# Optimization experiments

Hardware: AMD Instinct MI355X
Metric: run time of the kernel (lower is better)

Reference implementation:

```python
import jax, jax.numpy as jnp
import numpy as np

N, T, F, H, E, L = 50000, 12, 2, 64, 800000, 2


def setup_inputs() -> dict:
    key = jax.random.key(0)
    ks = jax.random.split(key, 8)
    x = jax.random.normal(ks[0], (N, T, F), jnp.float32)
    h0 = jnp.zeros((L, N, H), jnp.float32)
    edge_index = jax.random.randint(ks[1], (2, E), 0, N)
    edge_weight = jax.random.uniform(ks[2], (E,), jnp.float32)
    def glorot(k, shape):
        fan = shape[0]
        return jax.random.normal(k, shape, jnp.float32) / np.sqrt(fan).astype(np.float32)
    Wg0 = glorot(ks[3], (F + H, 2 * H)); bg0 = jnp.zeros((2 * H,), jnp.float32)
    Wc0 = glorot(ks[4], (F + H, H));     bc0 = jnp.zeros((H,), jnp.float32)
    Wg1 = glorot(ks[5], (H + H, 2 * H)); bg1 = jnp.zeros((2 * H,), jnp.float32)
    Wc1 = glorot(ks[6], (H + H, H));     bc1 = jnp.zeros((H,), jnp.float32)
    return dict(x=x, h0=h0, edge_index=edge_index, edge_weight=edge_weight,
                Wg0=Wg0, bg0=bg0, Wc0=Wc0, bc0=bc0,
                Wg1=Wg1, bg1=bg1, Wc1=Wc1, bc1=bc1)


def reference(x, h0, edge_index, edge_weight, Wg0, bg0, Wc0, bc0, Wg1, bg1, Wc1, bc1):
    n = x.shape[0]
    src, dst = edge_index[0], edge_index[1]

    def gcn(f, W, b):
        # weighted gather from src nodes, scatter-add into dst nodes, then linear
        agg = jax.ops.segment_sum(edge_weight[:, None] * f[src], dst, num_segments=n)
        return agg @ W + b

    def layer(inputs, h_init, Wg, bg, Wc, bc):
        def step(h, x_t):
            cat = jnp.concatenate([x_t, h], axis=-1)            # [N, F+H]
            zr = jax.nn.sigmoid(gcn(cat, Wg, bg))               # [N, 2H]
            z, r = jnp.split(zr, 2, axis=-1)
            cand = jnp.tanh(gcn(jnp.concatenate([x_t, r * h], axis=-1), Wc, bc))
            h_new = z * h + (1.0 - z) * cand
            return h_new, h_new
        hT, outs = jax.lax.scan(step, h_init, jnp.swapaxes(inputs, 0, 1))  # outs: [T, N, H]
        return hT, jnp.swapaxes(outs, 0, 1)                                # [N, T, H]

    h1, out1 = layer(x, h0[0], Wg0, bg0, Wc0, bc0)
    h2, out2 = layer(out1, h0[1], Wg1, bg1, Wc1, bc1)
    return jnp.stack([h1, h2], axis=0), out2
```

## Files before the change

### kernel.cpp

```cpp
#include <hip/hip_runtime.h>
#include <hip/hip_bf16.h>

#define DEV __device__ __forceinline__

DEV float4 ld4(const float* p) { return *reinterpret_cast<const float4*>(p); }
DEV float sigmoidf_(float x) { return 1.f / (1.f + expf(-x)); }

DEV void fma8(float (&a)[8], float xv, float4 wa, float4 wb) {
  a[0] = fmaf(xv, wa.x, a[0]); a[1] = fmaf(xv, wa.y, a[1]);
  a[2] = fmaf(xv, wa.z, a[2]); a[3] = fmaf(xv, wa.w, a[3]);
  a[4] = fmaf(xv, wb.x, a[4]); a[5] = fmaf(xv, wb.y, a[5]);
  a[6] = fmaf(xv, wb.z, a[6]); a[7] = fmaf(xv, wb.w, a[7]);
}
DEV void fma4(float (&a)[4], float xv, float4 wa) {
  a[0] = fmaf(xv, wa.x, a[0]); a[1] = fmaf(xv, wa.y, a[1]);
  a[2] = fmaf(xv, wa.z, a[2]); a[3] = fmaf(xv, wa.w, a[3]);
}
DEV float4 wfma4(float4 a, float w, float4 r) {
  a.x = __fadd_rn(a.x, __fmul_rn(w, r.x));
  a.y = __fadd_rn(a.y, __fmul_rn(w, r.y));
  a.z = __fadd_rn(a.z, __fmul_rn(w, r.z));
  a.w = __fadd_rn(a.w, __fmul_rn(w, r.w));
  return a;
}


__global__ void count_kernel(const int* __restrict__ dst, int* __restrict__ cnt, int E) {
  int e = blockIdx.x * blockDim.x + threadIdx.x;
  if (e < E) atomicAdd(&cnt[dst[e]], 1);
}

__global__ __launch_bounds__(256) void blockreduce_kernel(const int* __restrict__ cnt,
                                                          int* __restrict__ bsum, int n) {
  int i = blockIdx.x * 256 + threadIdx.x;
  int v = (i < n) ? cnt[i] : 0;
#pragma unroll
  for (int d = 1; d < 64; d <<= 1) v += __shfl_xor(v, d, 64);
  __shared__ int sh[4];
  if ((threadIdx.x & 63) == 0) sh[threadIdx.x >> 6] = v;
  __syncthreads();
  if (threadIdx.x == 0) bsum[blockIdx.x] = sh[0] + sh[1] + sh[2] + sh[3];
}

__global__ __launch_bounds__(256) void scanb_kernel(const int* __restrict__ bsum,
                                                    int* __restrict__ boff, int nb) {
  __shared__ int sh[256];
  int t = threadIdx.x;
  int orig = (t < nb) ? bsum[t] : 0;
  int v = orig;
  sh[t] = v;
  __syncthreads();
  for (int d = 1; d < 256; d <<= 1) {
    int a = (t >= d) ? sh[t - d] : 0;
    __syncthreads();
    v += a;
    sh[t] = v;
    __syncthreads();
  }
  if (t < nb) boff[t] = v - orig;
}

__global__ __launch_bounds__(256) void blockscan_kernel(
    const int* __restrict__ cnt, const int* __restrict__ boff,
    int* __restrict__ off, int* __restrict__ cur, int n, int total) {
  __shared__ int sh[256];
  int b = blockIdx.x, t = threadIdx.x;
  int i = b * 256 + t;
  int orig = (i < n) ? cnt[i] : 0;
  int v = orig;
  sh[t] = v;
  __syncthreads();
  for (int d = 1; d < 256; d <<= 1) {
    int a = (t >= d) ? sh[t - d] : 0;
    __syncthreads();
    v += a;
    sh[t] = v;
    __syncthreads();
  }
  int excl = v - orig + boff[b];
  if (i < n) { off[i] = excl; cur[i] = excl; }
  if (i == n - 1) off[n] = total;
}

__global__ void scatter_kernel(const int* __restrict__ dstI, int* __restrict__ cur,
                               int* __restrict__ eidx, int E) {
  int e = blockIdx.x * blockDim.x + threadIdx.x;
  if (e < E) {
    int p = atomicAdd(&cur[dstI[e]], 1);
    eidx[p] = e;
  }
}

__global__ __launch_bounds__(256) void sortseg_kernel(
    const int* __restrict__ off, int* __restrict__ eidx,
    const int* __restrict__ srcI, const float* __restrict__ ew,
    int2* __restrict__ cse, int n) {
  int node = blockIdx.x * 4 + (threadIdx.x >> 6);
  int lane = threadIdx.x & 63;
  if (node >= n) return;
  int s = off[node], e = off[node + 1];
  int deg = e - s;
  if (deg <= 0) return;
  if (deg <= 64) {
    int v = (lane < deg) ? eidx[s + lane] : 2147483647;
    int rank = 0;
    for (int m = 0; m < 64; ++m) {
      int u = __shfl(v, m, 64);
      rank += (u < v) ? 1 : 0;
    }
    if (lane < deg)
      cse[s + rank] = make_int2(srcI[v], __float_as_int(ew[v]));
  } else if (lane == 0) {
    for (int i = s + 1; i < e; ++i) {
      int key = eidx[i]; int j = i - 1;
      while (j >= s && eidx[j] > key) { eidx[j + 1] = eidx[j]; --j; }
      eidx[j + 1] = key;
    }
    for (int i = s; i < e; ++i) {
      int v = eidx[i];
      cse[i] = make_int2(srcI[v], __float_as_int(ew[v]));
    }
  }
}

__global__ __launch_bounds__(256) void aggx0_kernel(
    const int* __restrict__ off, const int2* __restrict__ cse,
    const float* __restrict__ x, float* __restrict__ ax, int n) {
  int node = blockIdx.x * 8 + (threadIdx.x >> 5);
  int lane = threadIdx.x & 31;
  if (node >= n || lane >= 24) return;
  float a = 0.f;
  int s = off[node], e = off[node + 1];
  int i = s;
  for (; i + 3 < e; i += 4) {
    int2 p0 = cse[i], p1 = cse[i + 1], p2 = cse[i + 2], p3 = cse[i + 3];
    float r0 = x[(size_t)p0.x * 24 + lane];
    float r1 = x[(size_t)p1.x * 24 + lane];
    float r2 = x[(size_t)p2.x * 24 + lane];
    float r3 = x[(size_t)p3.x * 24 + lane];
    a = __fadd_rn(a, __fmul_rn(__int_as_float(p0.y), r0));
    a = __fadd_rn(a, __fmul_rn(__int_as_float(p1.y), r1));
    a = __fadd_rn(a, __fmul_rn(__int_as_float(p2.y), r2));
    a = __fadd_rn(a, __fmul_rn(__int_as_float(p3.y), r3));
  }
  for (; i < e; ++i) {
    int2 p = cse[i];
    a = __fadd_rn(a, __fmul_rn(__int_as_float(p.y), x[(size_t)p.x * 24 + lane]));
  }
  ax[(size_t)node * 24 + lane] = a;
}


__global__ __launch_bounds__(256) void agg1_kernel(
    const int* __restrict__ off, const int2* __restrict__ cse,
    const float* __restrict__ f0, float* __restrict__ o0, int n) {
  const int node = blockIdx.x * 16 + (threadIdx.x >> 4);
  const int g4   = (threadIdx.x & 15) * 4;
  if (node >= n) return;
  int s = off[node], e = off[node + 1];
  float4 acc = make_float4(0.f, 0.f, 0.f, 0.f);
  int i = s;
  if (i + 3 < e) {
    int2 q0 = cse[i], q1 = cse[i + 1], q2 = cse[i + 2], q3 = cse[i + 3];
    for (; i + 7 < e; i += 4) {
      float4 r0 = ld4(f0 + (size_t)q0.x * 64 + g4);
      float4 r1 = ld4(f0 + (size_t)q1.x * 64 + g4);
      float4 r2 = ld4(f0 + (size_t)q2.x * 64 + g4);
      float4 r3 = ld4(f0 + (size_t)q3.x * 64 + g4);
      int2 m0 = cse[i + 4], m1 = cse[i + 5], m2 = cse[i + 6], m3 = cse[i + 7];
      acc = wfma4(acc, __int_as_float(q0.y), r0);
      acc = wfma4(acc, __int_as_float(q1.y), r1);
      acc = wfma4(acc, __int_as_float(q2.y), r2);
      acc = wfma4(acc, __int_as_float(q3.y), r3);
      q0 = m0; q1 = m1; q2 = m2; q3 = m3;
    }
    float4 r0 = ld4(f0 + (size_t)q0.x * 64 + g4);
    float4 r1 = ld4(f0 + (size_t)q1.x * 64 + g4);
    float4 r2 = ld4(f0 + (size_t)q2.x * 64 + g4);
    float4 r3 = ld4(f0 + (size_t)q3.x * 64 + g4);
    acc = wfma4(acc, __int_as_float(q0.y), r0);
    acc = wfma4(acc, __int_as_float(q1.y), r1);
    acc = wfma4(acc, __int_as_float(q2.y), r2);
    acc = wfma4(acc, __int_as_float(q3.y), r3);
    i += 4;
  }
  for (; i < e; ++i) {
    int2 p = cse[i];
    acc = wfma4(acc, __int_as_float(p.y), ld4(f0 + (size_t)p.x * 64 + g4));
  }
  *reinterpret_cast<float4*>(o0 + (size_t)node * 64 + g4) = acc;
}

__global__ __launch_bounds__(256) void agg2_kernel(
    const int* __restrict__ off, const int2* __restrict__ cse,
    const float* __restrict__ f0, float* __restrict__ o0,
    const float* __restrict__ f1, float* __restrict__ o1, int n) {
  const int node = blockIdx.x * 16 + (threadIdx.x >> 4);
  const int g4   = (threadIdx.x & 15) * 4;
  if (node >= n) return;
  int s = off[node], e = off[node + 1];
  float4 a0 = make_float4(0.f, 0.f, 0.f, 0.f);
  float4 a1 = a0;
  int i = s;
  if (i + 3 < e) {
    int2 q0 = cse[i], q1 = cse[i + 1], q2 = cse[i + 2], q3 = cse[i + 3];
    for (; i + 7 < e; i += 4) {
      size_t o0_ = (size_t)q0.x * 64 + g4, o1_ = (size_t)q1.x * 64 + g4;
      size_t o2_ = (size_t)q2.x * 64 + g4, o3_ = (size_t)q3.x * 64 + g4;
      float4 x0 = ld4(f0 + o0_), h0 = ld4(f1 + o0_);
      float4 x1 = ld4(f0 + o1_), h1 = ld4(f1 + o1_);
      float4 x2 = ld4(f0 + o2_), h2 = ld4(f1 + o2_);
      float4 x3 = ld4(f0 + o3_), h3 = ld4(f1 + o3_);
      int2 m0 = cse[i + 4], m1 = cse[i + 5], m2 = cse[i + 6], m3 = cse[i + 7];
      float w0 = __int_as_float(q0.y), w1 = __int_as_float(q1.y);
      float w2 = __int_as_float(q2.y), w3 = __int_as_float(q3.y);
      a0 = wfma4(a0, w0, x0); a1 = wfma4(a1, w0, h0);
      a0 = wfma4(a0, w1, x1); a1 = wfma4(a1, w1, h1);
      a0 = wfma4(a0, w2, x2); a1 = wfma4(a1, w2, h2);
      a0 = wfma4(a0, w3, x3); a1 = wfma4(a1, w3, h3);
      q0 = m0; q1 = m1; q2 = m2; q3 = m3;
    }
    size_t o0_ = (size_t)q0.x * 64 + g4, o1_ = (size_t)q1.x * 64 + g4;
    size_t o2_ = (size_t)q2.x * 64 + g4, o3_ = (size_t)q3.x * 64 + g4;
    float4 x0 = ld4(f0 + o0_), h0 = ld4(f1 + o0_);
    float4 x1 = ld4(f0 + o1_), h1 = ld4(f1 + o1_);
    float4 x2 = ld4(f0 + o2_), h2 = ld4(f1 + o2_);
    float4 x3 = ld4(f0 + o3_), h3 = ld4(f1 + o3_);
    float w0 = __int_as_float(q0.y), w1 = __int_as_float(q1.y);
    float w2 = __int_as_float(q2.y), w3 = __int_as_float(q3.y);
    a0 = wfma4(a0, w0, x0); a1 = wfma4(a1, w0, h0);
    a0 = wfma4(a0, w1, x1); a1 = wfma4(a1, w1, h1);
    a0 = wfma4(a0, w2, x2); a1 = wfma4(a1, w2, h2);
    a0 = wfma4(a0, w3, x3); a1 = wfma4(a1, w3, h3);
    i += 4;
  }
  for (; i < e; ++i) {
    int2 p = cse[i];
    float w = __int_as_float(p.y);
    size_t ro = (size_t)p.x * 64 + g4;
    a0 = wfma4(a0, w, ld4(f0 + ro));
    a1 = wfma4(a1, w, ld4(f1 + ro));
  }
  *reinterpret_cast<float4*>(o0 + (size_t)node * 64 + g4) = a0;
  *reinterpret_cast<float4*>(o1 + (size_t)node * 64 + g4) = a1;
}


template <int KX>
__global__ __launch_bounds__(256) void gates_kernel(
    const float* __restrict__ aggx, int sx,
    const float* __restrict__ aggh,
    const float* __restrict__ Wg, const float* __restrict__ bg,
    const float* __restrict__ hb, float* __restrict__ zb, float* __restrict__ rhb, int n) {
  __shared__ float wS[(KX + 64) * 128];
  const int t = threadIdx.x;
  {
    float4* d = (float4*)wS;
    const float4* src = (const float4*)Wg;
    const int tot = (KX + 64) * 32;
    for (int idx = t; idx < tot; idx += 256) d[idx] = src[idx];
  }
  __syncthreads();

  const int j0 = (t & 15) * 8;
  const int rb = blockIdx.x * 128 + (t >> 4) * 8;
  if (rb >= n) return;
  const int nr = min(8, n - rb);
  int ro[8];
#pragma unroll
  for (int r = 0; r < 8; ++r) ro[r] = (rb + (r < nr ? r : 0)) * 64;

  float a[8][8];
#pragma unroll
  for (int r = 0; r < 8; ++r)
#pragma unroll
    for (int i = 0; i < 8; ++i) a[r][i] = 0.f;

  {
    const float* Wh = wS + KX * 128;
    for (int k = 0; k < 64; k += 4) {
      float4 f[8];
#pragma unroll
      for (int r = 0; r < 8; ++r) f[r] = ld4(aggh + ro[r] + k);
#pragma unroll
      for (int kk = 0; kk < 4; ++kk) {
        const float* wr = Wh + (k + kk) * 128 + j0;
        float4 wa = ld4(wr), wb = ld4(wr + 4);
#pragma unroll
        for (int r = 0; r < 8; ++r) fma8(a[r], ((const float*)&f[r])[kk], wa, wb);
      }
    }
  }
  if constexpr (KX == 2) {
    float xv[8][2];
#pragma unroll
    for (int r = 0; r < 8; ++r) {
      size_t xo = (size_t)(rb + (r < nr ? r : 0)) * sx;
      xv[r][0] = aggx[xo]; xv[r][1] = aggx[xo + 1];
    }
#pragma unroll
    for (int k = 0; k < 2; ++k) {
      const float* wr = wS + k * 128 + j0;
      float4 wa = ld4(wr), wb = ld4(wr + 4);
#pragma unroll
      for (int r = 0; r < 8; ++r) fma8(a[r], xv[r][k], wa, wb);
    }
  } else {
    for (int k = 0; k < KX; k += 4) {
      float4 f[8];
#pragma unroll
      for (int r = 0; r < 8; ++r) f[r] = ld4(aggx + ro[r] + k);
#pragma unroll
      for (int kk = 0; kk < 4; ++kk) {
        const float* wr = wS + (k + kk) * 128 + j0;
        float4 wa = ld4(wr), wb = ld4(wr + 4);
#pragma unroll
        for (int r = 0; r < 8; ++r) fma8(a[r], ((const float*)&f[r])[kk], wa, wb);
      }
    }
  }
#pragma unroll
  for (int i = 0; i < 8; ++i) {
    int j = j0 + i;
    float b = bg[j];
#pragma unroll
    for (int r = 0; r < 8; ++r) {
      if (r < nr) {
        int row = rb + r;
        float sg = sigmoidf_(a[r][i] + b);
        if (j < 64) {
          zb[(size_t)row * 64 + j] = sg;
        } else {
          int jj = j - 64;
          rhb[(size_t)row * 64 + jj] = __fmul_rn(sg, hb[(size_t)row * 64 + jj]);
        }
      }
    }
  }
}


template <int KX>
__global__ __launch_bounds__(256) void cand_kernel(
    const float* __restrict__ aggx, int sx,
    const float* __restrict__ aggrh,
    const float* __restrict__ Wc, const float* __restrict__ bc,
    const float* __restrict__ zb, float* __restrict__ hb,
    float* __restrict__ outp, int ostride, int n) {
  __shared__ float wS[(KX + 64) * 64];
  const int t = threadIdx.x;
  {
    float4* d = (float4*)wS;
    const float4* src = (const float4*)Wc;
    const int tot = (KX + 64) * 16;
    for (int idx = t; idx < tot; idx += 256) d[idx] = src[idx];
  }
  __syncthreads();

  const int j0 = (t & 15) * 4;
  const int rb = blockIdx.x * 128 + (t >> 4) * 8;
  if (rb >= n) return;
  const int nr = min(8, n - rb);
  int ro[8];
#pragma unroll
  for (int r = 0; r < 8; ++r) ro[r] = (rb + (r < nr ? r : 0)) * 64;

  float a[8][4];
#pragma unroll
  for (int r = 0; r < 8; ++r)
#pragma unroll
    for (int i = 0; i < 4; ++i) a[r][i] = 0.f;

  {
    const float* Wh = wS + KX * 64;
    for (int k = 0; k < 64; k += 4) {
      float4 f[8];
#pragma unroll
      for (int r = 0; r < 8; ++r) f[r] = ld4(aggrh + ro[r] + k);
#pragma unroll
      for (int kk = 0; kk < 4; ++kk) {
        float4 wa = ld4(Wh + (k + kk) * 64 + j0);
#pragma unroll
        for (int r = 0; r < 8; ++r) fma4(a[r], ((const float*)&f[r])[kk], wa);
      }
    }
  }
  if constexpr (KX == 2) {
    float xv[8][2];
#pragma unroll
    for (int r = 0; r < 8; ++r) {
      size_t xo = (size_t)(rb + (r < nr ? r : 0)) * sx;
      xv[r][0] = aggx[xo]; xv[r][1] = aggx[xo + 1];
    }
#pragma unroll
    for (int k = 0; k < 2; ++k) {
      float4 wa = ld4(wS + k * 64 + j0);
#pragma unroll
      for (int r = 0; r < 8; ++r) fma4(a[r], xv[r][k], wa);
    }
  } else {
    for (int k = 0; k < KX; k += 4) {
      float4 f[8];
#pragma unroll
      for (int r = 0; r < 8; ++r) f[r] = ld4(aggx + ro[r] + k);
#pragma unroll
      for (int kk = 0; kk < 4; ++kk) {
        float4 wa = ld4(wS + (k + kk) * 64 + j0);
#pragma unroll
        for (int r = 0; r < 8; ++r) fma4(a[r], ((const float*)&f[r])[kk], wa);
      }
    }
  }
#pragma unroll
  for (int i = 0; i < 4; ++i) {
    int j = j0 + i;
    float b = bc[j];
#pragma unroll
    for (int r = 0; r < 8; ++r) {
      if (r < nr) {
        int row = rb + r;
        float c = tanhf(a[r][i] + b);
        float z = zb[(size_t)row * 64 + j];
        float h = hb[(size_t)row * 64 + j];
        float hn = __fadd_rn(__fmul_rn(z, h), __fmul_rn(1.f - z, c));
        hb[(size_t)row * 64 + j] = hn;
        outp[(size_t)row * ostride + j] = hn;
      }
    }
  }
}


extern "C" void kernel_launch(void* const* d_in, const int* in_sizes, int n_in,
                              void* d_out, int out_size, void* d_ws, size_t ws_size,
                              hipStream_t stream) {
  const float* x   = (const float*)d_in[0];
  const float* h0  = (const float*)d_in[1];
  const int*   ei  = (const int*)  d_in[2];
  const float* ew  = (const float*)d_in[3];
  const float* Wg0 = (const float*)d_in[4];
  const float* bg0 = (const float*)d_in[5];
  const float* Wc0 = (const float*)d_in[6];
  const float* bc0 = (const float*)d_in[7];
  const float* Wg1 = (const float*)d_in[8];
  const float* bg1 = (const float*)d_in[9];
  const float* Wc1 = (const float*)d_in[10];
  const float* bc1 = (const float*)d_in[11];

  const int N = in_sizes[0] / 24;
  const int E = in_sizes[2] / 2;
  const int NH = N * 64;
  const int NB = (N + 255) / 256;

  float* h1   = (float*)d_out;
  float* h2   = h1 + NH;
  float* out2 = h2 + NH;

  char* w = (char*)d_ws;
  auto alloc = [&](size_t bytes) {
    char* p = w;
    w += (bytes + 255) & ~(size_t)255;
    return p;
  };
  int*   cnt   = (int*)  alloc((size_t)N * 4);
  int*   off   = (int*)  alloc((size_t)(N + 1) * 4);
  int*   cur   = (int*)  alloc((size_t)N * 4);
  int2*  cse   = (int2*) alloc((size_t)E * 8);
  int*   bsum  = (int*)  alloc(256 * 4);
  int*   boff  = (int*)  alloc(256 * 4);
  float* aggx0 = (float*)alloc((size_t)N * 24 * 4);
  float* aggx1 = (float*)alloc((size_t)NH * 4);
  float* aggh  = (float*)alloc((size_t)NH * 4);
  float* aggrh = (float*)alloc((size_t)NH * 4);
  float* zb    = (float*)alloc((size_t)NH * 4);
  float* rhb   = (float*)alloc((size_t)NH * 4);
  float* o1t   = (float*)alloc((size_t)NH * 4);
  int*   eidx  = (int*)aggx1;

  const int* srcI = ei;
  const int* dstI = ei + E;

  hipMemcpyAsync(d_out, h0, (size_t)2 * NH * 4, hipMemcpyDeviceToDevice, stream);

  hipMemsetAsync(cnt, 0, (size_t)N * 4, stream);
  count_kernel<<<(E + 255) / 256, 256, 0, stream>>>(dstI, cnt, E);
  blockreduce_kernel<<<NB, 256, 0, stream>>>(cnt, bsum, N);
  scanb_kernel<<<1, 256, 0, stream>>>(bsum, boff, NB);
  blockscan_kernel<<<NB, 256, 0, stream>>>(cnt, boff, off, cur, N, E);
  scatter_kernel<<<(E + 255) / 256, 256, 0, stream>>>(dstI, cur, eidx, E);
  sortseg_kernel<<<(N + 3) / 4, 256, 0, stream>>>(off, eidx, srcI, ew, cse, N);

  aggx0_kernel<<<(N + 7) / 8, 256, 0, stream>>>(off, cse, x, aggx0, N);

  const int gagg = (N + 15) / 16;
  const int gmm  = (N + 127) / 128;

  for (int t = 0; t < 12; ++t) {
    agg1_kernel<<<gagg, 256, 0, stream>>>(off, cse, h1, aggh, N);
    gates_kernel<2><<<gmm, 256, 0, stream>>>(aggx0 + 2 * t, 24, aggh, Wg0, bg0, h1, zb, rhb, N);
    agg1_kernel<<<gagg, 256, 0, stream>>>(off, cse, rhb, aggrh, N);
    cand_kernel<2><<<gmm, 256, 0, stream>>>(aggx0 + 2 * t, 24, aggrh, Wc0, bc0, zb, h1, o1t, 64, N);
    agg2_kernel<<<gagg, 256, 0, stream>>>(off, cse, o1t, aggx1, h2, aggh, N);
    gates_kernel<64><<<gmm, 256, 0, stream>>>(aggx1, 64, aggh, Wg1, bg1, h2, zb, rhb, N);
    agg1_kernel<<<gagg, 256, 0, stream>>>(off, cse, rhb, aggrh, N);
    cand_kernel<64><<<gmm, 256, 0, stream>>>(aggx1, 64, aggrh, Wc1, bc1, zb, h2,
                                             out2 + (size_t)t * 64, 12 * 64, N);
  }
}
```

Measured before the change: 4.642 ms.

## Reorder aggregation nodes by in-degree to balance wavefront work

Builds a permutation of nodes sorted by clamped in-degree, using a per-block histogram, a scan and a placement pass, during preprocessing. The gather-aggregation kernels then process nodes in that order, so each wavefront holds nodes of similar degree and loses less time to divergence and tail imbalance. The cost is an extra indirection load per node, scattered output writes, lost locality of node ids, and a few extra setup kernels.

```diff
diff --git a/kernel.cpp b/kernel.cpp
--- a/kernel.cpp
+++ b/kernel.cpp
@@ -120,6 +120,37 @@
       int v = eidx[i];
       cse[i] = make_int2(srcI[v], __float_as_int(ew[v]));
     }
+  }
+}
+
+
+__global__ __launch_bounds__(256) void deghist_kernel(
+    const int* __restrict__ off, int* __restrict__ ghist, int n, int nb) {
+  __shared__ int h[256];
+  int t = threadIdx.x, b = blockIdx.x;
+  h[t] = 0;
+  __syncthreads();
+  int i = b * 256 + t;
+  if (i < n) {
+    int d = min(off[i + 1] - off[i], 255);
+    atomicAdd(&h[d], 1);
+  }
+  __syncthreads();
+  ghist[t * nb + b] = h[t];
+}
+
+__global__ __launch_bounds__(256) void degplace_kernel(
+    const int* __restrict__ off, const int* __restrict__ goff,
+    int* __restrict__ perm, int n, int nb) {
+  __shared__ int cur[256];
+  int t = threadIdx.x, b = blockIdx.x;
+  cur[t] = goff[t * nb + b];
+  __syncthreads();
+  int i = b * 256 + t;
+  if (i < n) {
+    int d = min(off[i + 1] - off[i], 255);
+    int pos = atomicAdd(&cur[d], 1);
+    perm[pos] = i;
   }
 }
 
@@ -153,10 +184,12 @@
 
 __global__ __launch_bounds__(256) void agg1_kernel(
     const int* __restrict__ off, const int2* __restrict__ cse,
+    const int* __restrict__ perm,
     const float* __restrict__ f0, float* __restrict__ o0, int n) {
-  const int node = blockIdx.x * 16 + (threadIdx.x >> 4);
-  const int g4   = (threadIdx.x & 15) * 4;
-  if (node >= n) return;
+  const int gi = blockIdx.x * 16 + (threadIdx.x >> 4);
+  const int g4 = (threadIdx.x & 15) * 4;
+  if (gi >= n) return;
+  const int node = perm[gi];
   int s = off[node], e = off[node + 1];
   float4 acc = make_float4(0.f, 0.f, 0.f, 0.f);
   int i = s;
@@ -193,11 +226,13 @@
 
 __global__ __launch_bounds__(256) void agg2_kernel(
     const int* __restrict__ off, const int2* __restrict__ cse,
+    const int* __restrict__ perm,
     const float* __restrict__ f0, float* __restrict__ o0,
     const float* __restrict__ f1, float* __restrict__ o1, int n) {
-  const int node = blockIdx.x * 16 + (threadIdx.x >> 4);
-  const int g4   = (threadIdx.x & 15) * 4;
-  if (node >= n) return;
+  const int gi = blockIdx.x * 16 + (threadIdx.x >> 4);
+  const int g4 = (threadIdx.x & 15) * 4;
+  if (gi >= n) return;
+  const int node = perm[gi];
   int s = off[node], e = off[node + 1];
   float4 a0 = make_float4(0.f, 0.f, 0.f, 0.f);
   float4 a1 = a0;
@@ -451,6 +486,8 @@
   const int E = in_sizes[2] / 2;
   const int NH = N * 64;
   const int NB = (N + 255) / 256;
+  const int NG = 256 * NB;
+  const int NB2 = (NG + 255) / 256;
 
   float* h1   = (float*)d_out;
   float* h2   = h1 + NH;
@@ -468,6 +505,10 @@
   int2*  cse   = (int2*) alloc((size_t)E * 8);
   int*   bsum  = (int*)  alloc(256 * 4);
   int*   boff  = (int*)  alloc(256 * 4);
+  int*   perm  = (int*)  alloc((size_t)N * 4);
+  int*   ghist = (int*)  alloc((size_t)NG * 4);
+  int*   goff  = (int*)  alloc((size_t)(NG + 1) * 4);
+  int*   gcur  = (int*)  alloc((size_t)NG * 4);
   float* aggx0 = (float*)alloc((size_t)N * 24 * 4);
   float* aggx1 = (float*)alloc((size_t)NH * 4);
   float* aggh  = (float*)alloc((size_t)NH * 4);
@@ -490,19 +531,25 @@
   scatter_kernel<<<(E + 255) / 256, 256, 0, stream>>>(dstI, cur, eidx, E);
   sortseg_kernel<<<(N + 3) / 4, 256, 0, stream>>>(off, eidx, srcI, ew, cse, N);
 
+  deghist_kernel<<<NB, 256, 0, stream>>>(off, ghist, N, NB);
+  blockreduce_kernel<<<NB2, 256, 0, stream>>>(ghist, bsum, NG);
+  scanb_kernel<<<1, 256, 0, stream>>>(bsum, boff, NB2);
+  blockscan_kernel<<<NB2, 256, 0, stream>>>(ghist, boff, goff, gcur, NG, N);
+  degplace_kernel<<<NB, 256, 0, stream>>>(off, goff, perm, N, NB);
+
   aggx0_kernel<<<(N + 7) / 8, 256, 0, stream>>>(off, cse, x, aggx0, N);
 
   const int gagg = (N + 15) / 16;
   const int gmm  = (N + 127) / 128;
 
   for (int t = 0; t < 12; ++t) {
-    agg1_kernel<<<gagg, 256, 0, stream>>>(off, cse, h1, aggh, N);
+    agg1_kernel<<<gagg, 256, 0, stream>>>(off, cse, perm, h1, aggh, N);
     gates_kernel<2><<<gmm, 256, 0, stream>>>(aggx0 + 2 * t, 24, aggh, Wg0, bg0, h1, zb, rhb, N);
-    agg1_kernel<<<gagg, 256, 0, stream>>>(off, cse, rhb, aggrh, N);
+    agg1_kernel<<<gagg, 256, 0, stream>>>(off, cse, perm, rhb, aggrh, N);
     cand_kernel<2><<<gmm, 256, 0, stream>>>(aggx0 + 2 * t, 24, aggrh, Wc0, bc0, zb, h1, o1t, 64, N);
-    agg2_kernel<<<gagg, 256, 0, stream>>>(off, cse, o1t, aggx1, h2, aggh, N);
+    agg2_kernel<<<gagg, 256, 0, stream>>>(off, cse, perm, o1t, aggx1, h2, aggh, N);
     gates_kernel<64><<<gmm, 256, 0, stream>>>(aggx1, 64, aggh, Wg1, bg1, h2, zb, rhb, N);
-    agg1_kernel<<<gagg, 256, 0, stream>>>(off, cse, rhb, aggrh, N);
+    agg1_kernel<<<gagg, 256, 0, stream>>>(off, cse, perm, rhb, aggrh, N);
     cand_kernel<64><<<gmm, 256, 0, stream>>>(aggx1, 64, aggrh, Wc1, bc1, zb, h2,
                                              out2 + (size_t)t * 64, 12 * 64, N);
   }
```

After: 4.723 ms. Within noise of the previous version (+1.8%).
